# Kernel tuning notes

Hardware: AMD Instinct MI355X
Metric: run time of the kernel (lower is better)

The kernel has to match this reference:

```python
import jax, jax.numpy as jnp
import numpy as np

B, A, G = 16, 262144, 128


def _make_boxes(key, shape):
    # boxes in (x1, y1, x2, y2) with strictly positive width/height
    k1, k2 = jax.random.split(key)
    cxy = jax.random.uniform(k1, shape[:-1] + (2,), minval=0.0, maxval=1024.0)
    wh = jax.random.uniform(k2, shape[:-1] + (2,), minval=8.0, maxval=256.0)
    return jnp.concatenate([cxy - 0.5 * wh, cxy + 0.5 * wh], axis=-1).astype(jnp.float32)


def setup_inputs() -> dict:
    key = jax.random.key(0)
    k1, k2, k3, k4 = jax.random.split(key, 4)
    bbox_regression = jax.random.normal(k1, (B, A, 4), dtype=jnp.float32)
    anchors = _make_boxes(k2, (A, 4))
    gt_boxes = _make_boxes(k3, (B, G, 4))
    # values in [-2, G): negatives are background/ignored, >=0 index into gt_boxes
    matched_idxs = jax.random.randint(k4, (B, A), -2, G, dtype=jnp.int32)
    return {
        "bbox_regression": bbox_regression,
        "anchors": anchors,
        "gt_boxes": gt_boxes,
        "matched_idxs": matched_idxs,
    }


def _encode(gt, anchors):
    # torchvision BoxCoder.encode_single with weights (1, 1, 1, 1)
    ex_w = anchors[..., 2] - anchors[..., 0]
    ex_h = anchors[..., 3] - anchors[..., 1]
    ex_cx = anchors[..., 0] + 0.5 * ex_w
    ex_cy = anchors[..., 1] + 0.5 * ex_h
    gt_w = gt[..., 2] - gt[..., 0]
    gt_h = gt[..., 3] - gt[..., 1]
    gt_cx = gt[..., 0] + 0.5 * gt_w
    gt_cy = gt[..., 1] + 0.5 * gt_h
    dx = (gt_cx - ex_cx) / ex_w
    dy = (gt_cy - ex_cy) / ex_h
    dw = jnp.log(gt_w / ex_w)
    dh = jnp.log(gt_h / ex_h)
    return jnp.stack([dx, dy, dw, dh], axis=-1)


def reference(bbox_regression, anchors, gt_boxes, matched_idxs):
    fg = matched_idxs >= 0                                  # [B, A] foreground mask
    idx = jnp.maximum(matched_idxs, 0)                      # clamp for safe gather
    matched_gt = jnp.take_along_axis(gt_boxes, idx[..., None], axis=1)  # [B, A, 4]
    target_regression = _encode(matched_gt, anchors[None, :, :])        # [B, A, 4]
    l1 = jnp.sum(jnp.abs(bbox_regression - target_regression), axis=-1)  # [B, A]
    l1 = jnp.where(fg, l1, 0.0)
    num_fg = jnp.sum(fg, axis=1)                            # [B]
    per_image = jnp.sum(l1, axis=1) / jnp.maximum(1, num_fg).astype(l1.dtype)
    return jnp.sum(per_image) / max(1, B)
```

## Files before the change

kernel.cpp:

```cpp
#include <hip/hip_runtime.h>
#include <math.h>

#define BB 16
#define AA 262144
#define GG 128
#define TPB 256
#define NBLK (AA / TPB)


__global__ __launch_bounds__(TPB, 4) void loss_main_kernel(
    const float4* __restrict__ reg,
    const float4* __restrict__ anc,
    const float4* __restrict__ gt,
    const int*   __restrict__ mi,
    float* __restrict__ ws_sum,
    float* __restrict__ ws_cnt)
{
    __shared__ float4 gts[BB * GG];
    __shared__ float redS[BB * 4];
    __shared__ float redC[BB * 4];

    const int t  = threadIdx.x;
    const int bx = blockIdx.x;

#pragma unroll
    for (int i = 0; i < (BB * GG) / TPB; ++i) {
        const float4 g = gt[i * TPB + t];
        const float w = g.z - g.x;
        const float h = g.w - g.y;
        gts[i * TPB + t] = make_float4(g.x + 0.5f * w, g.y + 0.5f * h,
                                       __logf(w), __logf(h));
    }
    __syncthreads();

    const int a = bx * TPB + t;
    const float4 an = anc[a];
    const float ex_w  = an.z - an.x;
    const float ex_h  = an.w - an.y;
    const float ex_cx = an.x + 0.5f * ex_w;
    const float ex_cy = an.y + 0.5f * ex_h;
    const float inv_w = 1.0f / ex_w;
    const float inv_h = 1.0f / ex_h;
    const float lw    = __logf(ex_w);
    const float lh    = __logf(ex_h);

    const int wv   = t >> 6;
    const int lane = t & 63;

#pragma unroll
    for (int b = 0; b < BB; ++b) {
        const int    mj = mi[b * AA + a];
        const float4 r  = reg[b * AA + a];
        const float4 g  = gts[b * GG + (mj < 0 ? 0 : mj)];

        const float dx = (g.x - ex_cx) * inv_w;
        const float dy = (g.y - ex_cy) * inv_h;
        const float dw = g.z - lw;
        const float dh = g.w - lh;

        const float l1 = fabsf(r.x - dx) + fabsf(r.y - dy) +
                         fabsf(r.z - dw) + fabsf(r.w - dh);
        float s = (mj >= 0) ? l1 : 0.0f;
        float c = (mj >= 0) ? 1.0f : 0.0f;

#pragma unroll
        for (int o = 32; o > 0; o >>= 1) {
            s += __shfl_down(s, o);
            c += __shfl_down(c, o);
        }
        if (lane == 0) { redS[b * 4 + wv] = s; redC[b * 4 + wv] = c; }
    }
    __syncthreads();

    if (t < BB) {
        const float s = redS[t * 4] + redS[t * 4 + 1] +
                        redS[t * 4 + 2] + redS[t * 4 + 3];
        const float c = redC[t * 4] + redC[t * 4 + 1] +
                        redC[t * 4 + 2] + redC[t * 4 + 3];
        ws_sum[t * NBLK + bx] = s;
        ws_cnt[t * NBLK + bx] = c;
    }
}

__global__ __launch_bounds__(TPB) void reduce_image_kernel(
    const float* __restrict__ ws_sum,
    const float* __restrict__ ws_cnt,
    float* __restrict__ per_img)
{
    __shared__ float redS[TPB / 64];
    __shared__ float redC[TPB / 64];
    const int b = blockIdx.x;
    const int t = threadIdx.x;

    float s = 0.0f, c = 0.0f;
    for (int i = t; i < NBLK; i += TPB) {
        s += ws_sum[b * NBLK + i];
        c += ws_cnt[b * NBLK + i];
    }
#pragma unroll
    for (int o = 32; o > 0; o >>= 1) {
        s += __shfl_down(s, o);
        c += __shfl_down(c, o);
    }
    const int lane = t & 63, wv = t >> 6;
    if (lane == 0) { redS[wv] = s; redC[wv] = c; }
    __syncthreads();
    if (t == 0) {
        float ss = 0.0f, cc = 0.0f;
#pragma unroll
        for (int i = 0; i < TPB / 64; ++i) { ss += redS[i]; cc += redC[i]; }
        per_img[b] = ss / fmaxf(1.0f, cc);
    }
}

__global__ void final_kernel(const float* __restrict__ per_img,
                             float* __restrict__ out)
{
    if (threadIdx.x == 0) {
        float acc = 0.0f;
#pragma unroll
        for (int b = 0; b < BB; ++b) acc += per_img[b];
        out[0] = acc / (float)BB;
    }
}

extern "C" void kernel_launch(void* const* d_in, const int* in_sizes, int n_in,
                              void* d_out, int out_size, void* d_ws, size_t ws_size,
                              hipStream_t stream) {
    const float4* reg = (const float4*)d_in[0];
    const float4* anc = (const float4*)d_in[1];
    const float4* gt  = (const float4*)d_in[2];
    const int*    mi  = (const int*)d_in[3];

    float* ws_sum  = (float*)d_ws;
    float* ws_cnt  = ws_sum + BB * NBLK;
    float* per_img = ws_cnt + BB * NBLK;

    loss_main_kernel<<<NBLK, TPB, 0, stream>>>(reg, anc, gt, mi, ws_sum, ws_cnt);
    reduce_image_kernel<<<BB, TPB, 0, stream>>>(ws_sum, ws_cnt, per_img);
    final_kernel<<<1, 64, 0, stream>>>(per_img, (float*)d_out);
}
```

Measured before the change: 120.3 us.

## Prefetch loads before barrier, ballot-count foregrounds, merge reduction kernels

The main kernel now issues all 16 matched-index loads before the shared-memory barrier, so they overlap the gt-table setup. Regression vectors are batched eight at a time to raise memory-level parallelism. The foreground count uses a ballot plus popcount instead of a second shuffle reduction. The per-image and final reduction kernels are merged into one single-block launch, which removes a launch but serialises 16 image reductions onto four waves and adds register pressure in the main kernel.

```diff
diff --git a/kernel.cpp b/kernel.cpp
--- a/kernel.cpp
+++ b/kernel.cpp
@@ -31,7 +31,6 @@
         gts[i * TPB + t] = make_float4(g.x + 0.5f * w, g.y + 0.5f * h,
                                        __logf(w), __logf(h));
     }
-    __syncthreads();
 
     const int a = bx * TPB + t;
     const float4 an = anc[a];
@@ -44,31 +43,46 @@
     const float lw    = __logf(ex_w);
     const float lh    = __logf(ex_h);
 
+    int mjv[BB];
+#pragma unroll
+    for (int b = 0; b < BB; ++b) mjv[b] = mi[b * AA + a];
+
+    __syncthreads();
+
     const int wv   = t >> 6;
     const int lane = t & 63;
 
 #pragma unroll
-    for (int b = 0; b < BB; ++b) {
-        const int    mj = mi[b * AA + a];
-        const float4 r  = reg[b * AA + a];
-        const float4 g  = gts[b * GG + (mj < 0 ? 0 : mj)];
-
-        const float dx = (g.x - ex_cx) * inv_w;
-        const float dy = (g.y - ex_cy) * inv_h;
-        const float dw = g.z - lw;
-        const float dh = g.w - lh;
-
-        const float l1 = fabsf(r.x - dx) + fabsf(r.y - dy) +
-                         fabsf(r.z - dw) + fabsf(r.w - dh);
-        float s = (mj >= 0) ? l1 : 0.0f;
-        float c = (mj >= 0) ? 1.0f : 0.0f;
+    for (int half = 0; half < 2; ++half) {
+        float4 r[8];
+#pragma unroll
+        for (int j = 0; j < 8; ++j)
+            r[j] = reg[(half * 8 + j) * AA + a];
 
 #pragma unroll
-        for (int o = 32; o > 0; o >>= 1) {
-            s += __shfl_down(s, o);
-            c += __shfl_down(c, o);
+        for (int j = 0; j < 8; ++j) {
+            const int b  = half * 8 + j;
+            const int mj = mjv[b];
+            const float4 g = gts[b * GG + (mj < 0 ? 0 : mj)];
+
+            const float dx = (g.x - ex_cx) * inv_w;
+            const float dy = (g.y - ex_cy) * inv_h;
+            const float dw = g.z - lw;
+            const float dh = g.w - lh;
+
+            const float l1 = fabsf(r[j].x - dx) + fabsf(r[j].y - dy) +
+                             fabsf(r[j].z - dw) + fabsf(r[j].w - dh);
+            float s = (mj >= 0) ? l1 : 0.0f;
+
+            const unsigned long long bal = __ballot(mj >= 0);
+#pragma unroll
+            for (int o = 32; o > 0; o >>= 1) s += __shfl_down(s, o);
+
+            if (lane == 0) {
+                redS[b * 4 + wv] = s;
+                redC[b * 4 + wv] = (float)__popcll(bal);
+            }
         }
-        if (lane == 0) { redS[b * 4 + wv] = s; redC[b * 4 + wv] = c; }
     }
     __syncthreads();
 
@@ -82,41 +96,35 @@
     }
 }
 
-__global__ __launch_bounds__(TPB) void reduce_image_kernel(
+__global__ __launch_bounds__(TPB) void reduce_final_kernel(
     const float* __restrict__ ws_sum,
     const float* __restrict__ ws_cnt,
-    float* __restrict__ per_img)
+    float* __restrict__ out)
 {
-    __shared__ float redS[TPB / 64];
-    __shared__ float redC[TPB / 64];
-    const int b = blockIdx.x;
-    const int t = threadIdx.x;
+    __shared__ float per_img[BB];
+    const int t    = threadIdx.x;
+    const int wv   = t >> 6;
+    const int lane = t & 63;
 
-    float s = 0.0f, c = 0.0f;
-    for (int i = t; i < NBLK; i += TPB) {
-        s += ws_sum[b * NBLK + i];
-        c += ws_cnt[b * NBLK + i];
+#pragma unroll
+    for (int k = 0; k < 4; ++k) {
+        const int b = wv * 4 + k;
+        float s = 0.0f, c = 0.0f;
+#pragma unroll
+        for (int i = 0; i < NBLK / 64; ++i) {
+            s += ws_sum[b * NBLK + i * 64 + lane];
+            c += ws_cnt[b * NBLK + i * 64 + lane];
+        }
+#pragma unroll
+        for (int o = 32; o > 0; o >>= 1) {
+            s += __shfl_down(s, o);
+            c += __shfl_down(c, o);
+        }
+        if (lane == 0) per_img[b] = s / fmaxf(1.0f, c);
     }
-#pragma unroll
-    for (int o = 32; o > 0; o >>= 1) {
-        s += __shfl_down(s, o);
-        c += __shfl_down(c, o);
-    }
-    const int lane = t & 63, wv = t >> 6;
-    if (lane == 0) { redS[wv] = s; redC[wv] = c; }
     __syncthreads();
+
     if (t == 0) {
-        float ss = 0.0f, cc = 0.0f;
-#pragma unroll
-        for (int i = 0; i < TPB / 64; ++i) { ss += redS[i]; cc += redC[i]; }
-        per_img[b] = ss / fmaxf(1.0f, cc);
-    }
-}
-
-__global__ void final_kernel(const float* __restrict__ per_img,
-                             float* __restrict__ out)
-{
-    if (threadIdx.x == 0) {
         float acc = 0.0f;
 #pragma unroll
         for (int b = 0; b < BB; ++b) acc += per_img[b];
@@ -132,11 +140,9 @@
     const float4* gt  = (const float4*)d_in[2];
     const int*    mi  = (const int*)d_in[3];
 
-    float* ws_sum  = (float*)d_ws;
-    float* ws_cnt  = ws_sum + BB * NBLK;
-    float* per_img = ws_cnt + BB * NBLK;
+    float* ws_sum = (float*)d_ws;
+    float* ws_cnt = ws_sum + BB * NBLK;
 
     loss_main_kernel<<<NBLK, TPB, 0, stream>>>(reg, anc, gt, mi, ws_sum, ws_cnt);
-    reduce_image_kernel<<<BB, TPB, 0, stream>>>(ws_sum, ws_cnt, per_img);
-    final_kernel<<<1, 64, 0, stream>>>(per_img, (float*)d_out);
+    reduce_final_kernel<<<1, TPB, 0, stream>>>(ws_sum, ws_cnt, (float*)d_out);
 }
```

Result: faster. 111.0 us, median of 2 (-7.7%).
